# Kernel tuning notes

Measured on AMD Instinct MI355X. Metric: run time of the kernel, lower is better.

Reference implementation:

```python
import jax, jax.numpy as jnp
import numpy as np

B, T, I, H, C = 8192, 28, 28, 128, 10


def setup_inputs() -> dict:
    key = jax.random.key(0)
    ks = jax.random.split(key, 7)
    s_ih = 1.0 / np.sqrt(H)
    return {
        "x": jax.random.normal(ks[0], (B, T, I), dtype=jnp.float32),
        "W_ih": jax.random.normal(ks[1], (4 * H, I), dtype=jnp.float32) * s_ih,
        "W_hh": jax.random.normal(ks[2], (4 * H, H), dtype=jnp.float32) * s_ih,
        "b_ih": jax.random.normal(ks[3], (4 * H,), dtype=jnp.float32) * s_ih,
        "b_hh": jax.random.normal(ks[4], (4 * H,), dtype=jnp.float32) * s_ih,
        "W_fc": jax.random.normal(ks[5], (C, H), dtype=jnp.float32) * s_ih,
        "b_fc": jnp.zeros((C,), dtype=jnp.float32),
    }


def reference(x, W_ih, W_hh, b_ih, b_hh, W_fc, b_fc):
    # x: [B, T, I]. PyTorch LSTM gate order: i, f, g, o.
    b = b_ih + b_hh  # [4H]
    # Precompute input projections for all timesteps: [T, B, 4H]
    x_proj = jnp.einsum("bti,gi->tbg", x, W_ih) + b
    h0 = jnp.zeros((x.shape[0], H), dtype=x.dtype)
    c0 = jnp.zeros_like(h0)

    def step(carry, xp_t):
        h, c = carry
        gates = xp_t + h @ W_hh.T  # [B, 4H]
        i_g, f_g, g_g, o_g = jnp.split(gates, 4, axis=-1)
        i_g = jax.nn.sigmoid(i_g)
        f_g = jax.nn.sigmoid(f_g)
        g_g = jnp.tanh(g_g)
        o_g = jax.nn.sigmoid(o_g)
        c = f_g * c + i_g * g_g
        h = o_g * jnp.tanh(c)
        return (h, c), None

    (h_last, _), _ = jax.lax.scan(step, (h0, c0), x_proj)
    # outputs[:, -1, :] == final hidden state; fc + relu
    return jax.nn.relu(h_last @ W_fc.T + b_fc)
```

## Files before the change

### kernel.cpp

```cpp
#include <hip/hip_runtime.h>
#include <math.h>

typedef __attribute__((ext_vector_type(8))) _Float16 half8;
typedef __attribute__((ext_vector_type(4))) _Float16 half4;
typedef __attribute__((ext_vector_type(4))) float    f32x4;
typedef __attribute__((ext_vector_type(2))) float    f32x2;

#define TSTEPS 28
#define IDIM   28
#define HDIM   128
#define NKC    5
#define TILE_B 16
#define CDIM   10

#if __has_builtin(__builtin_amdgcn_exp2f)
#define EXP2F(x) __builtin_amdgcn_exp2f(x)
#else
#define EXP2F(x) exp2f(x)
#endif
#if __has_builtin(__builtin_amdgcn_rcpf)
#define RCPF(x) __builtin_amdgcn_rcpf(x)
#else
#define RCPF(x) (1.0f / (x))
#endif

#define NLOG2E (-1.44269504f)
#define P2LOG2E (2.88539008f)

__global__ __launch_bounds__(256) void pack_w(const float* __restrict__ Wih,
                                              const float* __restrict__ Whh,
                                              const float* __restrict__ bih,
                                              const float* __restrict__ bhh,
                                              _Float16* __restrict__ P) {
    int e = blockIdx.x * 256 + threadIdx.x;
    if (e >= NKC * 4 * 8 * 64 * 8) return;
    int j  = e & 7;
    int ln = (e >> 3) & 63;
    int w  = (e >> 9) & 7;
    int t  = (e >> 12) & 3;
    int kc = e >> 14;
    int k  = kc * 32 + ((ln >> 4) << 3) + j;
    int u  = w * 16 + (ln & 15);
    int g  = t * HDIM + u;
    float v = 0.f;
    if (k < HDIM)                   v = Whh[g * HDIM + k];
    else if (k < HDIM + IDIM)       v = Wih[g * IDIM + (k - HDIM)];
    else if (k == HDIM + IDIM)      v = bih[g] + bhh[g];
    float sc = (t == 2) ? P2LOG2E : NLOG2E;
    P[e] = (_Float16)(v * sc);
}

__global__ __launch_bounds__(512, 2) void lstm_kernel(
    const float* __restrict__ x,
    const _Float16* __restrict__ P,
    const float* __restrict__ Wfc,
    const float* __restrict__ b_fc,
    float* __restrict__ out)
{
    __shared__ __align__(16) _Float16 frag[2][NKC][64][8];
    __shared__ __align__(16) _Float16 Plds[4][8][64][8];
    __shared__ __align__(16) float hplain[TILE_B][HDIM + 4];

    const int tid = threadIdx.x;
    const int l   = tid & 63;
    const int w   = tid >> 6;
    const int b0  = blockIdx.x * TILE_B;

    {
        const float4* P4 = (const float4*)P;
        float4* dst = (float4*)Plds;
        #pragma unroll
        for (int q = 0; q < 4; ++q)
            dst[tid + q * 512] = P4[8192 + tid + q * 512];
    }
    half8 breg[4][4];
    {
        const half8* Pp = (const half8*)P;
        #pragma unroll
        for (int kc = 0; kc < 4; ++kc)
            #pragma unroll
            for (int t4 = 0; t4 < 4; ++t4)
                breg[t4][kc] = Pp[((kc * 4 + t4) * 8 + w) * 64 + l];
    }

    if (tid < 256) {
        float4 z = {0.f, 0.f, 0.f, 0.f};
        ((float4*)&frag[0][0][0][0])[tid] = z;
    }
    if (tid < 32) {
        int b = tid >> 4, i = tid & 15;
        half4 onev = {(_Float16)1.f, (_Float16)0.f, (_Float16)0.f, (_Float16)0.f};
        *(half4*)&frag[b][4][48 + i][4] = onev;
    }
    const int xrow = tid / 7, xg = tid % 7;
    const int xslot = (tid < 112) ? (xrow + 16 * (xg >> 1)) : 0;
    const int xoff  = (xg & 1) * 4;
    if (tid < 112) {
        const float4* xs = (const float4*)(x + (size_t)(b0 + xrow) * (TSTEPS * IDIM));
        float4 x0 = xs[xg];
        float4 x1 = xs[7 + xg];
        half4 h0 = {(_Float16)x0.x, (_Float16)x0.y, (_Float16)x0.z, (_Float16)x0.w};
        half4 h1 = {(_Float16)x1.x, (_Float16)x1.y, (_Float16)x1.z, (_Float16)x1.w};
        *(half4*)&frag[0][4][xslot][xoff] = h0;
        *(half4*)&frag[1][4][xslot][xoff] = h1;
    }

    f32x2 cst01 = {0.f, 0.f}, cst23 = {0.f, 0.f};
    const int u    = w * 16 + (l & 15);
    const int kc_h = w >> 1;
    const int quad = (2 * w + ((l >> 3) & 1)) & 3;
    const int jh   = l & 7;
    const int mb   = (l >> 4) << 2;

    __syncthreads();

#if __has_builtin(__builtin_amdgcn_s_sleep)
    if (blockIdx.x & 256) __builtin_amdgcn_s_sleep(32);
#endif

    f32x4 acc[4];
    auto zero_acc = [&]() {
        #pragma unroll
        for (int t4 = 0; t4 < 4; ++t4) { f32x4 z = {0.f, 0.f, 0.f, 0.f}; acc[t4] = z; }
    };
    auto kc4_mfma = [&](half8 a4) {
        #pragma unroll
        for (int t4 = 0; t4 < 4; ++t4) {
            half8 b = *(const half8*)&Plds[t4][w][l][0];
            acc[t4] = __builtin_amdgcn_mfma_f32_16x16x32_f16(a4, b, acc[t4], 0, 0, 0);
        }
    };

    zero_acc();
    kc4_mfma(*(const half8*)&frag[0][4][l][0]);

    for (int t = 0; t < TSTEPS; ++t) {
        const _Float16 (*cur)[64][8] = frag[t & 1];
        _Float16 (*nxt)[64][8] = frag[(t & 1) ^ 1];
        const bool last   = (t == TSTEPS - 1);
        const bool doload = (t + 2 < TSTEPS) && (tid < 112);

        float4 xv;
        if (doload)
            xv = ((const float4*)(x + (size_t)(b0 + xrow) * (TSTEPS * IDIM)))[(t + 2) * 7 + xg];

        half8 a[4];
        #pragma unroll
        for (int kc = 0; kc < 4; ++kc)
            a[kc] = *(const half8*)&cur[kc][l][0];
        #pragma unroll
        for (int t4 = 0; t4 < 4; ++t4)
            #pragma unroll
            for (int kc = 0; kc < 4; ++kc)
                acc[t4] = __builtin_amdgcn_mfma_f32_16x16x32_f16(a[kc], breg[t4][kc], acc[t4], 0, 0, 0);

        half8 a4n;
        if (!last) a4n = *(const half8*)&nxt[4][l][0];

        float hv[4];
        #pragma unroll
        for (int rp = 0; rp < 2; ++rp) {
            const int r0 = rp * 2, r1 = r0 + 1;
            f32x2 Ei = {EXP2F(acc[0][r0]), EXP2F(acc[0][r1])};
            f32x2 Ef = {EXP2F(acc[1][r0]), EXP2F(acc[1][r1])};
            f32x2 Eg = {EXP2F(acc[2][r0]), EXP2F(acc[2][r1])};
            f32x2 Eo = {EXP2F(acc[3][r0]), EXP2F(acc[3][r1])};
            f32x2 one = {1.f, 1.f};
            f32x2 Di = Ei + one, Df = Ef + one, Dg = Eg + one, Do = Eo + one;
            f32x2 Pif = Di * Df, Pgo = Dg * Do;
            f32x2 Rif = {RCPF(Pif.x), RCPF(Pif.y)};
            f32x2 Rgo = {RCPF(Pgo.x), RCPF(Pgo.y)};
            f32x2 is = Rif * Df, fs = Rif * Di;
            f32x2 gt = one - 2.f * (Rgo * Do);
            f32x2 os = Rgo * Dg;
            f32x2 cstp = rp ? cst23 : cst01;
            f32x2 c = fs * cstp + is * gt;
            if (rp) cst23 = c; else cst01 = c;
            f32x2 Etc = {EXP2F(c.x * P2LOG2E), EXP2F(c.y * P2LOG2E)};
            f32x2 Dtc = Etc + one;
            f32x2 Rtc = {RCPF(Dtc.x), RCPF(Dtc.y)};
            f32x2 tc = one - 2.f * Rtc;
            f32x2 h2 = os * tc;
            hv[r0] = h2.x; hv[r1] = h2.y;
        }

        #pragma unroll
        for (int r = 0; r < 4; ++r) {
            nxt[kc_h][mb + r + 16 * quad][jh] = (_Float16)hv[r];
            if (last) hplain[mb + r][u] = hv[r];
        }

        if (!last) {
            zero_acc();
            kc4_mfma(a4n);
        }
        if (doload) {
            half4 hc = {(_Float16)xv.x, (_Float16)xv.y, (_Float16)xv.z, (_Float16)xv.w};
            *(half4*)&((_Float16 (*)[64][8])cur)[4][xslot][xoff] = hc;
        }
        __syncthreads();
    }

    if (tid < TILE_B * CDIM) {
        int row = tid / CDIM, c = tid % CDIM;
        const float4* hv4 = (const float4*)&hplain[row][0];
        const float4* wf  = (const float4*)(Wfc + c * HDIM);
        float s = b_fc[c];
        #pragma unroll
        for (int q = 0; q < 32; ++q) {
            float4 a4 = hv4[q], b4 = wf[q];
            s += a4.x * b4.x + a4.y * b4.y + a4.z * b4.z + a4.w * b4.w;
        }
        out[(size_t)(b0 + row) * CDIM + c] = fmaxf(s, 0.f);
    }
}

extern "C" void kernel_launch(void* const* d_in, const int* in_sizes, int n_in,
                              void* d_out, int out_size, void* d_ws, size_t ws_size,
                              hipStream_t stream) {
    const float* x   = (const float*)d_in[0];
    const float* Wih = (const float*)d_in[1];
    const float* Whh = (const float*)d_in[2];
    const float* bih = (const float*)d_in[3];
    const float* bhh = (const float*)d_in[4];
    const float* Wfc = (const float*)d_in[5];
    const float* bfc = (const float*)d_in[6];
    float* out = (float*)d_out;
    _Float16* P = (_Float16*)d_ws;

    hipLaunchKernelGGL(pack_w, dim3(320), dim3(256), 0, stream, Wih, Whh, bih, bhh, P);
    hipLaunchKernelGGL(lstm_kernel, dim3(8192 / TILE_B), dim3(512), 0, stream,
                       x, P, Wfc, bfc, out);
}
```

Before: 122.6 us.

## Interleave two batch sub-tiles per block to overlap MFMA with activations

```diff
diff --git a/kernel.cpp b/kernel.cpp
--- a/kernel.cpp
+++ b/kernel.cpp
@@ -10,7 +10,7 @@
 #define IDIM   28
 #define HDIM   128
 #define NKC    5
-#define TILE_B 16
+#define TILE_B 32
 #define CDIM   10
 
 #if __has_builtin(__builtin_amdgcn_exp2f)
@@ -58,7 +58,6 @@
     float* __restrict__ out)
 {
     __shared__ __align__(16) _Float16 frag[2][NKC][64][8];
-    __shared__ __align__(16) _Float16 Plds[4][8][64][8];
     __shared__ __align__(16) float hplain[TILE_B][HDIM + 4];
 
     const int tid = threadIdx.x;
@@ -66,14 +65,8 @@
     const int w   = tid >> 6;
     const int b0  = blockIdx.x * TILE_B;
 
-    {
-        const float4* P4 = (const float4*)P;
-        float4* dst = (float4*)Plds;
-        #pragma unroll
-        for (int q = 0; q < 4; ++q)
-            dst[tid + q * 512] = P4[8192 + tid + q * 512];
-    }
     half8 breg[4][4];
+    half8 breg4[4];
     {
         const half8* Pp = (const half8*)P;
         #pragma unroll
@@ -81,90 +74,62 @@
             #pragma unroll
             for (int t4 = 0; t4 < 4; ++t4)
                 breg[t4][kc] = Pp[((kc * 4 + t4) * 8 + w) * 64 + l];
-    }
-
-    if (tid < 256) {
+        #pragma unroll
+        for (int t4 = 0; t4 < 4; ++t4)
+            breg4[t4] = Pp[((4 * 4 + t4) * 8 + w) * 64 + l];
+    }
+
+    {
         float4 z = {0.f, 0.f, 0.f, 0.f};
-        ((float4*)&frag[0][0][0][0])[tid] = z;
+        if (tid < 256) {
+            ((float4*)frag)[tid] = z;
+            ((float4*)frag)[320 + tid] = z;
+        }
     }
     if (tid < 32) {
-        int b = tid >> 4, i = tid & 15;
+        int g = tid >> 4, i = tid & 15;
         half4 onev = {(_Float16)1.f, (_Float16)0.f, (_Float16)0.f, (_Float16)0.f};
-        *(half4*)&frag[b][4][48 + i][4] = onev;
-    }
-    const int xrow = tid / 7, xg = tid % 7;
-    const int xslot = (tid < 112) ? (xrow + 16 * (xg >> 1)) : 0;
+        *(half4*)&frag[g][4][48 + i][4] = onev;
+    }
+
+    const bool xact = (l < 14);
+    const int xid   = w * 14 + l;
+    const int xrow  = xid / 7, xg = xid % 7;
+    const int xslot = xrow + 16 * (xg >> 1);
     const int xoff  = (xg & 1) * 4;
-    if (tid < 112) {
-        const float4* xs = (const float4*)(x + (size_t)(b0 + xrow) * (TSTEPS * IDIM));
-        float4 x0 = xs[xg];
-        float4 x1 = xs[7 + xg];
-        half4 h0 = {(_Float16)x0.x, (_Float16)x0.y, (_Float16)x0.z, (_Float16)x0.w};
-        half4 h1 = {(_Float16)x1.x, (_Float16)x1.y, (_Float16)x1.z, (_Float16)x1.w};
-        *(half4*)&frag[0][4][xslot][xoff] = h0;
-        *(half4*)&frag[1][4][xslot][xoff] = h1;
-    }
-
-    f32x2 cst01 = {0.f, 0.f}, cst23 = {0.f, 0.f};
+    const float4* xsA = (const float4*)(x + (size_t)(b0 + xrow) * (TSTEPS * IDIM));
+    const float4* xsB = (const float4*)(x + (size_t)(b0 + 16 + xrow) * (TSTEPS * IDIM));
+    float4 xh;
+    if (xact) {
+        float4 xa0 = xsA[xg];
+        float4 xb0 = xsB[xg];
+        half4 ha = {(_Float16)xa0.x, (_Float16)xa0.y, (_Float16)xa0.z, (_Float16)xa0.w};
+        half4 hb = {(_Float16)xb0.x, (_Float16)xb0.y, (_Float16)xb0.z, (_Float16)xb0.w};
+        *(half4*)&frag[0][4][xslot][xoff] = ha;
+        *(half4*)&frag[1][4][xslot][xoff] = hb;
+        xh = xsA[7 + xg];
+    }
+
+    f32x2 cA01 = {0.f, 0.f}, cA23 = {0.f, 0.f};
+    f32x2 cB01 = {0.f, 0.f}, cB23 = {0.f, 0.f};
     const int u    = w * 16 + (l & 15);
     const int kc_h = w >> 1;
     const int quad = (2 * w + ((l >> 3) & 1)) & 3;
     const int jh   = l & 7;
     const int mb   = (l >> 4) << 2;
 
-    __syncthreads();
-
-#if __has_builtin(__builtin_amdgcn_s_sleep)
-    if (blockIdx.x & 256) __builtin_amdgcn_s_sleep(32);
-#endif
-
-    f32x4 acc[4];
-    auto zero_acc = [&]() {
-        #pragma unroll
-        for (int t4 = 0; t4 < 4; ++t4) { f32x4 z = {0.f, 0.f, 0.f, 0.f}; acc[t4] = z; }
-    };
-    auto kc4_mfma = [&](half8 a4) {
-        #pragma unroll
-        for (int t4 = 0; t4 < 4; ++t4) {
-            half8 b = *(const half8*)&Plds[t4][w][l][0];
-            acc[t4] = __builtin_amdgcn_mfma_f32_16x16x32_f16(a4, b, acc[t4], 0, 0, 0);
-        }
-    };
-
-    zero_acc();
-    kc4_mfma(*(const half8*)&frag[0][4][l][0]);
-
-    for (int t = 0; t < TSTEPS; ++t) {
-        const _Float16 (*cur)[64][8] = frag[t & 1];
-        _Float16 (*nxt)[64][8] = frag[(t & 1) ^ 1];
-        const bool last   = (t == TSTEPS - 1);
-        const bool doload = (t + 2 < TSTEPS) && (tid < 112);
-
-        float4 xv;
-        if (doload)
-            xv = ((const float4*)(x + (size_t)(b0 + xrow) * (TSTEPS * IDIM)))[(t + 2) * 7 + xg];
-
-        half8 a[4];
-        #pragma unroll
-        for (int kc = 0; kc < 4; ++kc)
-            a[kc] = *(const half8*)&cur[kc][l][0];
-        #pragma unroll
-        for (int t4 = 0; t4 < 4; ++t4)
-            #pragma unroll
-            for (int kc = 0; kc < 4; ++kc)
-                acc[t4] = __builtin_amdgcn_mfma_f32_16x16x32_f16(a[kc], breg[t4][kc], acc[t4], 0, 0, 0);
-
-        half8 a4n;
-        if (!last) a4n = *(const half8*)&nxt[4][l][0];
-
+    f32x4 acc_A[4], acc_B[4];
+
+    auto activation = [&](f32x4 (&g4)[4], f32x2 &c01, f32x2 &c23,
+                          _Float16 (*fragA)[64][8], bool lastT, int rowbase) {
         float hv[4];
         #pragma unroll
         for (int rp = 0; rp < 2; ++rp) {
             const int r0 = rp * 2, r1 = r0 + 1;
-            f32x2 Ei = {EXP2F(acc[0][r0]), EXP2F(acc[0][r1])};
-            f32x2 Ef = {EXP2F(acc[1][r0]), EXP2F(acc[1][r1])};
-            f32x2 Eg = {EXP2F(acc[2][r0]), EXP2F(acc[2][r1])};
-            f32x2 Eo = {EXP2F(acc[3][r0]), EXP2F(acc[3][r1])};
+            f32x2 Ei = {EXP2F(g4[0][r0]), EXP2F(g4[0][r1])};
+            f32x2 Ef = {EXP2F(g4[1][r0]), EXP2F(g4[1][r1])};
+            f32x2 Eg = {EXP2F(g4[2][r0]), EXP2F(g4[2][r1])};
+            f32x2 Eo = {EXP2F(g4[3][r0]), EXP2F(g4[3][r1])};
             f32x2 one = {1.f, 1.f};
             f32x2 Di = Ei + one, Df = Ef + one, Dg = Eg + one, Do = Eo + one;
             f32x2 Pif = Di * Df, Pgo = Dg * Do;
@@ -173,9 +138,9 @@
             f32x2 is = Rif * Df, fs = Rif * Di;
             f32x2 gt = one - 2.f * (Rgo * Do);
             f32x2 os = Rgo * Dg;
-            f32x2 cstp = rp ? cst23 : cst01;
+            f32x2 cstp = rp ? c23 : c01;
             f32x2 c = fs * cstp + is * gt;
-            if (rp) cst23 = c; else cst01 = c;
+            if (rp) c23 = c; else c01 = c;
             f32x2 Etc = {EXP2F(c.x * P2LOG2E), EXP2F(c.y * P2LOG2E)};
             f32x2 Dtc = Etc + one;
             f32x2 Rtc = {RCPF(Dtc.x), RCPF(Dtc.y)};
@@ -183,23 +148,74 @@
             f32x2 h2 = os * tc;
             hv[r0] = h2.x; hv[r1] = h2.y;
         }
-
         #pragma unroll
         for (int r = 0; r < 4; ++r) {
-            nxt[kc_h][mb + r + 16 * quad][jh] = (_Float16)hv[r];
-            if (last) hplain[mb + r][u] = hv[r];
-        }
-
-        if (!last) {
-            zero_acc();
-            kc4_mfma(a4n);
-        }
-        if (doload) {
-            half4 hc = {(_Float16)xv.x, (_Float16)xv.y, (_Float16)xv.z, (_Float16)xv.w};
-            *(half4*)&((_Float16 (*)[64][8])cur)[4][xslot][xoff] = hc;
-        }
+            fragA[kc_h][mb + r + 16 * quad][jh] = (_Float16)hv[r];
+            if (lastT) hplain[rowbase + mb + r][u] = hv[r];
+        }
+    };
+
+    auto run_phase = [&](f32x4 (&accM)[4], _Float16 (*fragM)[64][8],
+                         f32x4 (&accA)[4], _Float16 (*fragA)[64][8],
+                         f32x2 &c01, f32x2 &c23, int rowbase,
+                         bool doAct, bool doKc4, bool lastT) {
+        half8 a[4];
+        #pragma unroll
+        for (int kc = 0; kc < 4; ++kc)
+            a[kc] = *(const half8*)&fragM[kc][l][0];
+        half8 a4;
+        if (doKc4) a4 = *(const half8*)&fragA[4][l][0];
+        #pragma unroll
+        for (int t4 = 0; t4 < 4; ++t4)
+            #pragma unroll
+            for (int kc = 0; kc < 4; ++kc)
+                accM[t4] = __builtin_amdgcn_mfma_f32_16x16x32_f16(a[kc], breg[t4][kc], accM[t4], 0, 0, 0);
+        if (doAct) activation(accA, c01, c23, fragA, lastT, rowbase);
+        if (doKc4) {
+            #pragma unroll
+            for (int t4 = 0; t4 < 4; ++t4) { f32x4 z = {0.f, 0.f, 0.f, 0.f}; accA[t4] = z; }
+            #pragma unroll
+            for (int t4 = 0; t4 < 4; ++t4)
+                accA[t4] = __builtin_amdgcn_mfma_f32_16x16x32_f16(a4, breg4[t4], accA[t4], 0, 0, 0);
+        }
+    };
+
+    __syncthreads();
+
+    {
+        half8 aA4 = *(const half8*)&frag[0][4][l][0];
+        #pragma unroll
+        for (int t4 = 0; t4 < 4; ++t4) { f32x4 z = {0.f, 0.f, 0.f, 0.f}; acc_A[t4] = z; }
+        #pragma unroll
+        for (int t4 = 0; t4 < 4; ++t4)
+            acc_A[t4] = __builtin_amdgcn_mfma_f32_16x16x32_f16(aA4, breg4[t4], acc_A[t4], 0, 0, 0);
+    }
+    __syncthreads();
+
+    for (int t = 0; t < TSTEPS; ++t) {
+        const bool more = (t + 1 < TSTEPS);
+
+        if (xact && more) {
+            half4 hc = {(_Float16)xh.x, (_Float16)xh.y, (_Float16)xh.z, (_Float16)xh.w};
+            *(half4*)&frag[0][4][xslot][xoff] = hc;
+        }
+        run_phase(acc_A, frag[0], acc_B, frag[1], cB01, cB23, 16,
+                  t > 0, true, false);
+        if (xact && more) xh = xsB[(t + 1) * 7 + xg];
         __syncthreads();
-    }
+
+        if (xact && more) {
+            half4 hc = {(_Float16)xh.x, (_Float16)xh.y, (_Float16)xh.z, (_Float16)xh.w};
+            *(half4*)&frag[1][4][xslot][xoff] = hc;
+        }
+        run_phase(acc_B, frag[1], acc_A, frag[0], cA01, cA23, 0,
+                  true, more, !more);
+        if (xact && t + 2 < TSTEPS) xh = xsA[(t + 2) * 7 + xg];
+        __syncthreads();
+    }
+
+    activation(acc_B, cB01, cB23, frag[1], true, 16);
+    __syncthreads();
 
     if (tid < TILE_B * CDIM) {
         int row = tid / CDIM, c = tid % CDIM;
```

Result: slower. 130.2 us (+6.2%).

## Ping-pong two 16-row sub-tiles so MFMA and activation phases overlap

Applied to the files above, without the earlier changes.

```diff
diff --git a/kernel.cpp b/kernel.cpp
--- a/kernel.cpp
+++ b/kernel.cpp
@@ -10,7 +10,7 @@
 #define IDIM   28
 #define HDIM   128
 #define NKC    5
-#define TILE_B 16
+#define TILE_B 32
 #define CDIM   10
 
 #if __has_builtin(__builtin_amdgcn_exp2f)
@@ -23,9 +23,16 @@
 #else
 #define RCPF(x) (1.0f / (x))
 #endif
+#if __has_builtin(__builtin_amdgcn_s_setprio)
+#define SETPRIO(p) __builtin_amdgcn_s_setprio(p)
+#else
+#define SETPRIO(p)
+#endif
 
 #define NLOG2E (-1.44269504f)
 #define P2LOG2E (2.88539008f)
+
+#define MFMA16(a,b,c) __builtin_amdgcn_mfma_f32_16x16x32_f16((a),(b),(c),0,0,0)
 
 __global__ __launch_bounds__(256) void pack_w(const float* __restrict__ Wih,
                                               const float* __restrict__ Whh,
@@ -58,146 +65,143 @@
     float* __restrict__ out)
 {
     __shared__ __align__(16) _Float16 frag[2][NKC][64][8];
-    __shared__ __align__(16) _Float16 Plds[4][8][64][8];
     __shared__ __align__(16) float hplain[TILE_B][HDIM + 4];
 
     const int tid = threadIdx.x;
     const int l   = tid & 63;
     const int w   = tid >> 6;
+    const int sid = w >> 2;
+    const int w4  = w & 3;
     const int b0  = blockIdx.x * TILE_B;
 
-    {
-        const float4* P4 = (const float4*)P;
-        float4* dst = (float4*)Plds;
-        #pragma unroll
-        for (int q = 0; q < 4; ++q)
-            dst[tid + q * 512] = P4[8192 + tid + q * 512];
-    }
-    half8 breg[4][4];
+    half8 breg[4][2][4];
+    half8 breg4[4][2];
     {
         const half8* Pp = (const half8*)P;
         #pragma unroll
-        for (int kc = 0; kc < 4; ++kc)
+        for (int g = 0; g < 4; ++g)
             #pragma unroll
-            for (int t4 = 0; t4 < 4; ++t4)
-                breg[t4][kc] = Pp[((kc * 4 + t4) * 8 + w) * 64 + l];
-    }
-
-    if (tid < 256) {
+            for (int n = 0; n < 2; ++n) {
+                #pragma unroll
+                for (int kc = 0; kc < 4; ++kc)
+                    breg[g][n][kc] = Pp[((kc * 4 + g) * 8 + (2 * w4 + n)) * 64 + l];
+                breg4[g][n] = Pp[((4 * 4 + g) * 8 + (2 * w4 + n)) * 64 + l];
+            }
+    }
+
+    {
         float4 z = {0.f, 0.f, 0.f, 0.f};
-        ((float4*)&frag[0][0][0][0])[tid] = z;
+        ((float4*)frag)[(tid < 256) ? tid : (tid + 64)] = z;
     }
     if (tid < 32) {
-        int b = tid >> 4, i = tid & 15;
+        int s = tid >> 4, i = tid & 15;
         half4 onev = {(_Float16)1.f, (_Float16)0.f, (_Float16)0.f, (_Float16)0.f};
-        *(half4*)&frag[b][4][48 + i][4] = onev;
-    }
-    const int xrow = tid / 7, xg = tid % 7;
-    const int xslot = (tid < 112) ? (xrow + 16 * (xg >> 1)) : 0;
+        *(half4*)&frag[s][4][48 + i][4] = onev;
+    }
+
+    const int xid   = tid & 255;
+    const bool xact = (xid < 112);
+    const int xrow  = xid / 7, xg = xid % 7;
+    const int xslot = xrow + 16 * (xg >> 1);
     const int xoff  = (xg & 1) * 4;
-    if (tid < 112) {
-        const float4* xs = (const float4*)(x + (size_t)(b0 + xrow) * (TSTEPS * IDIM));
-        float4 x0 = xs[xg];
-        float4 x1 = xs[7 + xg];
+    const float4* xs4 = (const float4*)(x + (size_t)(b0 + sid * 16 + xrow) * (TSTEPS * IDIM));
+    float4 xh;
+    if (xact) {
+        float4 x0 = xs4[xg];
         half4 h0 = {(_Float16)x0.x, (_Float16)x0.y, (_Float16)x0.z, (_Float16)x0.w};
-        half4 h1 = {(_Float16)x1.x, (_Float16)x1.y, (_Float16)x1.z, (_Float16)x1.w};
-        *(half4*)&frag[0][4][xslot][xoff] = h0;
-        *(half4*)&frag[1][4][xslot][xoff] = h1;
-    }
-
-    f32x2 cst01 = {0.f, 0.f}, cst23 = {0.f, 0.f};
-    const int u    = w * 16 + (l & 15);
-    const int kc_h = w >> 1;
-    const int quad = (2 * w + ((l >> 3) & 1)) & 3;
-    const int jh   = l & 7;
-    const int mb   = (l >> 4) << 2;
-
-    __syncthreads();
-
-#if __has_builtin(__builtin_amdgcn_s_sleep)
-    if (blockIdx.x & 256) __builtin_amdgcn_s_sleep(32);
-#endif
-
-    f32x4 acc[4];
-    auto zero_acc = [&]() {
-        #pragma unroll
-        for (int t4 = 0; t4 < 4; ++t4) { f32x4 z = {0.f, 0.f, 0.f, 0.f}; acc[t4] = z; }
+        *(half4*)&frag[sid][4][xslot][xoff] = h0;
+    }
+
+    const int l15 = l & 15;
+    const int mb  = (l >> 4) << 2;
+    const int jh  = l & 7;
+    const int q0  = (l >> 3) & 1;
+    _Float16 (*myfrag)[64][8] = frag[sid];
+
+    f32x4 acc[4][2];
+    f32x2 cst[4];
+    cst[0] = cst[1] = cst[2] = cst[3] = (f32x2){0.f, 0.f};
+    const f32x4 zc = {0.f, 0.f, 0.f, 0.f};
+
+    auto mfma_phase = [&](int t) {
+        if (xact && t + 1 < TSTEPS) xh = xs4[(t + 1) * 7 + xg];
+        half8 a0 = *(const half8*)&myfrag[0][l][0];
+        half8 a1 = *(const half8*)&myfrag[1][l][0];
+        half8 a2 = *(const half8*)&myfrag[2][l][0];
+        half8 a3 = *(const half8*)&myfrag[3][l][0];
+        half8 a4 = *(const half8*)&myfrag[4][l][0];
+        SETPRIO(1);
+        #pragma unroll
+        for (int g = 0; g < 4; ++g)
+            #pragma unroll
+            for (int n = 0; n < 2; ++n) {
+                f32x4 c = MFMA16(a4, breg4[g][n], zc);
+                c = MFMA16(a0, breg[g][n][0], c);
+                c = MFMA16(a1, breg[g][n][1], c);
+                c = MFMA16(a2, breg[g][n][2], c);
+                c = MFMA16(a3, breg[g][n][3], c);
+                acc[g][n] = c;
+            }
+        SETPRIO(0);
     };
-    auto kc4_mfma = [&](half8 a4) {
-        #pragma unroll
-        for (int t4 = 0; t4 < 4; ++t4) {
-            half8 b = *(const half8*)&Plds[t4][w][l][0];
-            acc[t4] = __builtin_amdgcn_mfma_f32_16x16x32_f16(a4, b, acc[t4], 0, 0, 0);
+
+    auto act_phase = [&](int t) {
+        const bool lastT = (t == TSTEPS - 1);
+        #pragma unroll
+        for (int n = 0; n < 2; ++n) {
+            float hv[4];
+            #pragma unroll
+            for (int rp = 0; rp < 2; ++rp) {
+                const int r0 = rp * 2, r1 = r0 + 1;
+                f32x2 Ei = {EXP2F(acc[0][n][r0]), EXP2F(acc[0][n][r1])};
+                f32x2 Ef = {EXP2F(acc[1][n][r0]), EXP2F(acc[1][n][r1])};
+                f32x2 Eg = {EXP2F(acc[2][n][r0]), EXP2F(acc[2][n][r1])};
+                f32x2 Eo = {EXP2F(acc[3][n][r0]), EXP2F(acc[3][n][r1])};
+                f32x2 one = {1.f, 1.f};
+                f32x2 Di = Ei + one, Df = Ef + one, Dg = Eg + one, Do = Eo + one;
+                f32x2 Pif = Di * Df, Pgo = Dg * Do;
+                f32x2 Rif = {RCPF(Pif.x), RCPF(Pif.y)};
+                f32x2 Rgo = {RCPF(Pgo.x), RCPF(Pgo.y)};
+                f32x2 is = Rif * Df, fs = Rif * Di;
+                f32x2 gt = one - 2.f * (Rgo * Do);
+                f32x2 os = Rgo * Dg;
+                f32x2 c = fs * cst[2 * n + rp] + is * gt;
+                cst[2 * n + rp] = c;
+                f32x2 Etc = {EXP2F(c.x * P2LOG2E), EXP2F(c.y * P2LOG2E)};
+                f32x2 Dtc = Etc + one;
+                f32x2 Rtc = {RCPF(Dtc.x), RCPF(Dtc.y)};
+                f32x2 tc = one - 2.f * Rtc;
+                f32x2 h2 = os * tc;
+                hv[r0] = h2.x; hv[r1] = h2.y;
+            }
+            if (lastT) {
+                #pragma unroll
+                for (int r = 0; r < 4; ++r)
+                    hplain[sid * 16 + mb + r][32 * w4 + n * 16 + l15] = hv[r];
+            } else {
+                const int qn = q0 + 2 * n;
+                #pragma unroll
+                for (int r = 0; r < 4; ++r)
+                    myfrag[w4][mb + r + 16 * qn][jh] = (_Float16)hv[r];
+            }
+        }
+        if (xact && t + 1 < TSTEPS) {
+            half4 hc = {(_Float16)xh.x, (_Float16)xh.y, (_Float16)xh.z, (_Float16)xh.w};
+            *(half4*)&myfrag[4][xslot][xoff] = hc;
         }
     };
 
-    zero_acc();
-    kc4_mfma(*(const half8*)&frag[0][4][l][0]);
+    __syncthreads();
+
+    if (sid == 0) mfma_phase(0);
+    __syncthreads();
 
     for (int t = 0; t < TSTEPS; ++t) {
-        const _Float16 (*cur)[64][8] = frag[t & 1];
-        _Float16 (*nxt)[64][8] = frag[(t & 1) ^ 1];
-        const bool last   = (t == TSTEPS - 1);
-        const bool doload = (t + 2 < TSTEPS) && (tid < 112);
-
-        float4 xv;
-        if (doload)
-            xv = ((const float4*)(x + (size_t)(b0 + xrow) * (TSTEPS * IDIM)))[(t + 2) * 7 + xg];
-
-        half8 a[4];
-        #pragma unroll
-        for (int kc = 0; kc < 4; ++kc)
-            a[kc] = *(const half8*)&cur[kc][l][0];
-        #pragma unroll
-        for (int t4 = 0; t4 < 4; ++t4)
-            #pragma unroll
-            for (int kc = 0; kc < 4; ++kc)
-                acc[t4] = __builtin_amdgcn_mfma_f32_16x16x32_f16(a[kc], breg[t4][kc], acc[t4], 0, 0, 0);
-
-        half8 a4n;
-        if (!last) a4n = *(const half8*)&nxt[4][l][0];
-
-        float hv[4];
-        #pragma unroll
-        for (int rp = 0; rp < 2; ++rp) {
-            const int r0 = rp * 2, r1 = r0 + 1;
-            f32x2 Ei = {EXP2F(acc[0][r0]), EXP2F(acc[0][r1])};
-            f32x2 Ef = {EXP2F(acc[1][r0]), EXP2F(acc[1][r1])};
-            f32x2 Eg = {EXP2F(acc[2][r0]), EXP2F(acc[2][r1])};
-            f32x2 Eo = {EXP2F(acc[3][r0]), EXP2F(acc[3][r1])};
-            f32x2 one = {1.f, 1.f};
-            f32x2 Di = Ei + one, Df = Ef + one, Dg = Eg + one, Do = Eo + one;
-            f32x2 Pif = Di * Df, Pgo = Dg * Do;
-            f32x2 Rif = {RCPF(Pif.x), RCPF(Pif.y)};
-            f32x2 Rgo = {RCPF(Pgo.x), RCPF(Pgo.y)};
-            f32x2 is = Rif * Df, fs = Rif * Di;
-            f32x2 gt = one - 2.f * (Rgo * Do);
-            f32x2 os = Rgo * Dg;
-            f32x2 cstp = rp ? cst23 : cst01;
-            f32x2 c = fs * cstp + is * gt;
-            if (rp) cst23 = c; else cst01 = c;
-            f32x2 Etc = {EXP2F(c.x * P2LOG2E), EXP2F(c.y * P2LOG2E)};
-            f32x2 Dtc = Etc + one;
-            f32x2 Rtc = {RCPF(Dtc.x), RCPF(Dtc.y)};
-            f32x2 tc = one - 2.f * Rtc;
-            f32x2 h2 = os * tc;
-            hv[r0] = h2.x; hv[r1] = h2.y;
-        }
-
-        #pragma unroll
-        for (int r = 0; r < 4; ++r) {
-            nxt[kc_h][mb + r + 16 * quad][jh] = (_Float16)hv[r];
-            if (last) hplain[mb + r][u] = hv[r];
-        }
-
-        if (!last) {
-            zero_acc();
-            kc4_mfma(a4n);
-        }
-        if (doload) {
-            half4 hc = {(_Float16)xv.x, (_Float16)xv.y, (_Float16)xv.z, (_Float16)xv.w};
-            *(half4*)&((_Float16 (*)[64][8])cur)[4][xslot][xoff] = hc;
-        }
+        if (sid == 0) act_phase(t);
+        else          mfma_phase(t);
+        __syncthreads();
+        if (sid == 0) { if (t + 1 < TSTEPS) mfma_phase(t + 1); }
+        else          act_phase(t);
         __syncthreads();
     }
 
```

Result: slower. 132.6 us (+8.2%).
